# Kernel tuning notes

Measured on AMD Instinct MI355X. Metric: run time of the kernel, lower is better.

Reference implementation:

```python
import jax, jax.numpy as jnp
import numpy as np

N, E, D_IN, HEADS, C = 100000, 1600000, 128, 4, 32  # C = out_channels per head


def setup_inputs() -> dict:
    key = jax.random.key(0)
    ks = jax.random.split(key, 10)
    s = 1.0 / np.sqrt(D_IN)
    return {
        "x": jax.random.normal(ks[0], (N, D_IN), jnp.float32),
        "edge_index": jax.random.randint(ks[1], (2, E), 0, N, jnp.int64),
        "Wq": jax.random.normal(ks[2], (D_IN, HEADS * C), jnp.float32) * s,
        "bq": jnp.zeros((HEADS * C,), jnp.float32),
        "Wk": jax.random.normal(ks[3], (D_IN, HEADS * C), jnp.float32) * s,
        "bk": jnp.zeros((HEADS * C,), jnp.float32),
        "Wv": jax.random.normal(ks[4], (D_IN, HEADS * C), jnp.float32) * s,
        "bv": jnp.zeros((HEADS * C,), jnp.float32),
        "Wskip": jax.random.normal(ks[5], (D_IN, HEADS * C), jnp.float32) * s,
        "bskip": jnp.zeros((HEADS * C,), jnp.float32),
    }


def reference(x, edge_index, Wq, bq, Wk, bk, Wv, bv, Wskip, bskip):
    n = x.shape[0]
    src, dst = edge_index[0], edge_index[1]  # message flows src (j) -> dst (i)
    q = (x @ Wq + bq).reshape(n, HEADS, C)
    k = (x @ Wk + bk).reshape(n, HEADS, C)
    v = (x @ Wv + bv).reshape(n, HEADS, C)

    # per-edge attention logits [E, H]
    alpha = jnp.einsum('ehc,ehc->eh', q[dst], k[src]) / jnp.sqrt(jnp.float32(C))

    # segment softmax over incoming edges of each target node
    m = jax.ops.segment_max(alpha, dst, num_segments=n)          # [N, H]
    p = jnp.exp(alpha - m[dst])                                   # [E, H]
    z = jax.ops.segment_sum(p, dst, num_segments=n)               # [N, H]
    w = p / (z[dst] + 1e-16)                                      # [E, H]

    # softmax-weighted scatter aggregation of values
    out = jax.ops.segment_sum(v[src] * w[:, :, None], dst, num_segments=n)
    out = out.reshape(n, HEADS * C)

    # root/skip connection (beta=False default: plain add)
    out = out + x @ Wskip + bskip
    return out
```

## Files before the change

kernel.cpp:

```cpp
#include <hip/hip_runtime.h>

#define DIN 128
#define NHEADS 4
#define CH 32
#define MT 128
#define CHUNK 4096
#define NPB 256
#define EPB_IT 25

#define ST_H 136

typedef _Float16 h8 __attribute__((ext_vector_type(8)));
typedef _Float16 h2 __attribute__((ext_vector_type(2)));
typedef float f4 __attribute__((ext_vector_type(4)));
typedef unsigned int u2v __attribute__((ext_vector_type(2)));

__global__ __launch_bounds__(256) void prep_w(
    const float* __restrict__ Wq, const float* __restrict__ Wk,
    const float* __restrict__ Wv, const float* __restrict__ Wsk,
    _Float16* __restrict__ wt)
{
    int i = blockIdx.x * 256 + threadIdx.x;
    if (i >= 4 * 16384) return;
    int mat = i >> 14;
    int rem = i & 16383;
    int n  = rem >> 7;
    int kk = rem & 127;
    const float* W = (mat == 0) ? Wq : (mat == 1) ? Wk : (mat == 2) ? Wv : Wsk;
    wt[i] = (_Float16)W[kk * 128 + n];
}

__global__ __launch_bounds__(256) void qkvs_all(
    const float* __restrict__ x, const _Float16* __restrict__ wt,
    const float* __restrict__ bq, const float* __restrict__ bk,
    const float* __restrict__ bv, const float* __restrict__ bsk,
    _Float16* __restrict__ qh, _Float16* __restrict__ kvh,
    _Float16* __restrict__ skiph, int N)
{
    __shared__ _Float16 Sbuf[17408];
    const int t = threadIdx.x;
    const int rowBase = blockIdx.x * MT;

    for (int i = t; i < MT * 16; i += 256) {
        int r  = i >> 4;
        int c8 = i & 15;
        int gr = rowBase + r;
        _Float16 h[8];
        if (gr < N) {
            float4 f0 = reinterpret_cast<const float4*>(x)[(size_t)gr * 32 + c8 * 2];
            float4 f1 = reinterpret_cast<const float4*>(x)[(size_t)gr * 32 + c8 * 2 + 1];
            h[0] = (_Float16)f0.x; h[1] = (_Float16)f0.y;
            h[2] = (_Float16)f0.z; h[3] = (_Float16)f0.w;
            h[4] = (_Float16)f1.x; h[5] = (_Float16)f1.y;
            h[6] = (_Float16)f1.z; h[7] = (_Float16)f1.w;
        } else {
            #pragma unroll
            for (int j = 0; j < 8; ++j) h[j] = (_Float16)0.f;
        }
        *reinterpret_cast<uint4*>(&Sbuf[r * 128 + ((c8 ^ (r & 7)) << 3)]) =
            *reinterpret_cast<uint4*>(h);
    }
    __syncthreads();

    const int wid  = t >> 6;
    const int l    = t & 63;
    const int lm   = l & 15;
    const int quad = l >> 4;

    h8 afrag[2][4];
    #pragma unroll
    for (int kq = 0; kq < 4; ++kq) {
        int c8 = kq * 4 + quad;
        afrag[0][kq] = *reinterpret_cast<const h8*>(
            &Sbuf[(wid * 32 + lm) * 128 + ((c8 ^ (lm & 7)) << 3)]);
        afrag[1][kq] = *reinterpret_cast<const h8*>(
            &Sbuf[(wid * 32 + 16 + lm) * 128 + ((c8 ^ (lm & 7)) << 3)]);
    }
    __syncthreads();

    for (int mat = 0; mat < 4; ++mat) {
        const _Float16* __restrict__ Bsrc = wt + (size_t)mat * 16384;

        f4 acc[2][8];
        #pragma unroll
        for (int ms = 0; ms < 2; ++ms)
            #pragma unroll
            for (int nt = 0; nt < 8; ++nt)
                acc[ms][nt] = (f4){0.f, 0.f, 0.f, 0.f};

        #pragma unroll
        for (int kq = 0; kq < 4; ++kq) {
            const int k0 = (kq * 4 + quad) << 3;
            #pragma unroll
            for (int nt = 0; nt < 8; ++nt) {
                h8 b = *reinterpret_cast<const h8*>(
                    &Bsrc[(size_t)(nt * 16 + lm) * 128 + k0]);
                acc[0][nt] = __builtin_amdgcn_mfma_f32_16x16x32_f16(afrag[0][kq], b, acc[0][nt], 0, 0, 0);
                acc[1][nt] = __builtin_amdgcn_mfma_f32_16x16x32_f16(afrag[1][kq], b, acc[1][nt], 0, 0, 0);
            }
        }

        const float* bias = (mat == 0) ? bq : (mat == 1) ? bk : (mat == 2) ? bv : bsk;

        #pragma unroll
        for (int ms = 0; ms < 2; ++ms) {
            #pragma unroll
            for (int nt = 0; nt < 8; ++nt) {
                int col = nt * 16 + lm;
                float bsv = bias[col];
                int row = wid * 32 + ms * 16 + quad * 4;
                #pragma unroll
                for (int i2 = 0; i2 < 4; ++i2)
                    Sbuf[(row + i2) * ST_H + col] = (_Float16)(acc[ms][nt][i2] + bsv);
            }
        }
        __syncthreads();
        if (mat == 0 || mat == 3) {
            _Float16* __restrict__ dst = (mat == 0) ? qh : skiph;
            for (int j = t; j < 2048; j += 256) {
                int r  = j >> 4;
                int c0 = (j & 15) << 3;
                int gr = rowBase + r;
                if (gr < N)
                    *reinterpret_cast<uint4*>(&dst[(size_t)gr * 128 + c0]) =
                        *reinterpret_cast<const uint4*>(&Sbuf[r * ST_H + c0]);
            }
        } else {
            const int koff = (mat == 2) ? 4 : 0;
            for (int j = t; j < 4096; j += 256) {
                int r = j >> 5;
                int g = j & 31;
                int gr = rowBase + r;
                if (gr < N)
                    *reinterpret_cast<uint2*>(&kvh[(size_t)gr * 256 + g * 8 + koff]) =
                        *reinterpret_cast<const uint2*>(&Sbuf[r * ST_H + g * 4]);
            }
        }
        __syncthreads();
    }
}

__global__ __launch_bounds__(256) void bucket_hist(
    const int* __restrict__ ei, int* __restrict__ bcnt, int E, int nb)
{
    __shared__ int lds[512];
    for (int b = threadIdx.x; b < nb; b += 256) lds[b] = 0;
    __syncthreads();
    for (long long i = (long long)blockIdx.x * 256 + threadIdx.x; i < E;
         i += (long long)gridDim.x * 256)
        atomicAdd(&lds[ei[(size_t)E + i] >> 8], 1);
    __syncthreads();
    for (int b = threadIdx.x; b < nb; b += 256)
        if (lds[b]) atomicAdd(&bcnt[b], lds[b]);
}

__global__ __launch_bounds__(512) void scan_buckets(
    const int* __restrict__ bcnt, int* __restrict__ boff,
    int* __restrict__ bcur, int nb)
{
    __shared__ int ws[8];
    int t = threadIdx.x, lane = t & 63, wid = t >> 6;
    int v = (t < nb) ? bcnt[t] : 0;
    int s = v;
    #pragma unroll
    for (int off = 1; off < 64; off <<= 1) {
        int n = __shfl_up(s, off);
        if (lane >= off) s += n;
    }
    if (lane == 63) ws[wid] = s;
    __syncthreads();
    int add = 0;
    for (int w = 0; w < wid; ++w) add += ws[w];
    int excl = s - v + add;
    if (t < nb) { boff[t] = excl; bcur[t] = excl; }
    if (t == nb - 1) boff[nb] = excl + v;
}

__global__ __launch_bounds__(256) void bucket_scatter(
    const int* __restrict__ ei, int* __restrict__ bcur,
    uint2* __restrict__ pairs, int E, int nb)
{
    __shared__ int cnt[512];
    int t = threadIdx.x;
    for (int b = t; b < nb; b += 256) cnt[b] = 0;
    __syncthreads();

    long long e0 = (long long)blockIdx.x * (256 * EPB_IT);
    int ps[EPB_IT], pd[EPB_IT];
    #pragma unroll
    for (int j = 0; j < EPB_IT; ++j) {
        long long e = e0 + j * 256 + t;
        if (e < E) {
            ps[j] = ei[e];
            pd[j] = ei[(size_t)E + e];
            atomicAdd(&cnt[pd[j] >> 8], 1);
        } else pd[j] = -1;
    }
    __syncthreads();
    for (int b = t; b < nb; b += 256) {
        int c = cnt[b];
        if (c) cnt[b] = atomicAdd(&bcur[b], c);
    }
    __syncthreads();
    #pragma unroll
    for (int j = 0; j < EPB_IT; ++j) {
        if (pd[j] >= 0) {
            int pos = atomicAdd(&cnt[pd[j] >> 8], 1);
            pairs[pos] = make_uint2((unsigned)ps[j], (unsigned)pd[j]);
        }
    }
}

__global__ __launch_bounds__(256) void bucket_counts(
    const uint2* __restrict__ pairs, const int* __restrict__ boff,
    int* __restrict__ counts, int N)
{
    __shared__ int cnt[NPB];
    int b = blockIdx.x, t = threadIdx.x;
    cnt[t] = 0;
    __syncthreads();
    int s = boff[b], e = boff[b + 1];
    for (int i = s + t; i < e; i += 256)
        atomicAdd(&cnt[pairs[i].y & (NPB - 1)], 1);
    __syncthreads();
    int node = b * NPB + t;
    if (node < N) counts[node] = cnt[t];
}

__global__ __launch_bounds__(256) void chunk_sums(
    const int* __restrict__ counts, int* __restrict__ partials, int N)
{
    int b = blockIdx.x, t = threadIdx.x;
    int base = b * CHUNK + t * 16;
    int s = 0;
    #pragma unroll
    for (int j = 0; j < 16; ++j) {
        int i = base + j;
        if (i < N) s += counts[i];
    }
    #pragma unroll
    for (int off = 1; off < 64; off <<= 1) s += __shfl_xor(s, off);
    __shared__ int ws[4];
    int lane = t & 63, wid = t >> 6;
    if (lane == 0) ws[wid] = s;
    __syncthreads();
    if (t == 0) partials[b] = ws[0] + ws[1] + ws[2] + ws[3];
}

__global__ __launch_bounds__(256) void scan_chunks(
    const int* __restrict__ partials, int* __restrict__ chunkoff, int nch)
{
    __shared__ int ws[4];
    int t = threadIdx.x, lane = t & 63, wid = t >> 6;
    int v = (t < nch) ? partials[t] : 0;
    int s = v;
    #pragma unroll
    for (int off = 1; off < 64; off <<= 1) {
        int n = __shfl_up(s, off);
        if (lane >= off) s += n;
    }
    if (lane == 63) ws[wid] = s;
    __syncthreads();
    int add = 0;
    for (int w = 0; w < wid; ++w) add += ws[w];
    if (t < nch) chunkoff[t] = s - v + add;
}

__global__ __launch_bounds__(256) void scan_write(
    const int* __restrict__ counts, const int* __restrict__ chunkoff,
    int* __restrict__ rowptr, int N)
{
    int b = blockIdx.x, t = threadIdx.x;
    int base = b * CHUNK + t * 16;
    int vals[16];
    int s = 0;
    #pragma unroll
    for (int j = 0; j < 16; ++j) {
        int i = base + j;
        vals[j] = (i < N) ? counts[i] : 0;
        s += vals[j];
    }
    int lane = t & 63, wid = t >> 6;
    int incl = s;
    #pragma unroll
    for (int off = 1; off < 64; off <<= 1) {
        int n = __shfl_up(incl, off);
        if (lane >= off) incl += n;
    }
    __shared__ int ws[4];
    if (lane == 63) ws[wid] = incl;
    __syncthreads();
    int add = chunkoff[b];
    for (int w = 0; w < wid; ++w) add += ws[w];
    int run = incl - s + add;
    #pragma unroll
    for (int j = 0; j < 16; ++j) {
        int i = base + j;
        if (i < N) rowptr[i + 1] = run + vals[j];
        run += vals[j];
    }
    if (b == 0 && t == 0) rowptr[0] = 0;
}

__global__ __launch_bounds__(256) void bucket_place(
    const uint2* __restrict__ pairs, const int* __restrict__ boff,
    const int* __restrict__ rowptr, int* __restrict__ sorted, int N)
{
    __shared__ int cur[NPB];
    int b = blockIdx.x, t = threadIdx.x;
    int node = b * NPB + t;
    cur[t] = (node < N) ? rowptr[node] : 0;
    __syncthreads();
    int s = boff[b], e = boff[b + 1];
    for (int i = s + t; i < e; i += 256) {
        uint2 pr = pairs[i];
        int pos = atomicAdd(&cur[pr.y & (NPB - 1)], 1);
        sorted[pos] = (int)pr.x;
    }
}

__device__ inline float4 cvt4(unsigned lo, unsigned hi) {
    union { unsigned u[2]; _Float16 h[4]; } c;
    c.u[0] = lo; c.u[1] = hi;
    return make_float4((float)c.h[0], (float)c.h[1], (float)c.h[2], (float)c.h[3]);
}

__device__ inline h2 as_h2(unsigned u) {
    union { unsigned u; h2 h; } c;
    c.u = u;
    return c.h;
}

__global__ __launch_bounds__(256) void node_aggregate(
    const _Float16* __restrict__ q, const _Float16* __restrict__ kv,
    const _Float16* __restrict__ skiph,
    const int* __restrict__ rowptr, const int* __restrict__ srcs,
    float* __restrict__ out, int N)
{
    int gid  = blockIdx.x * 256 + threadIdx.x;
    int node = gid >> 5;
    if (node >= N) return;
    int l = gid & 31;

    u2v qu = __builtin_nontemporal_load(
        reinterpret_cast<const u2v*>(q + (size_t)node * 128) + l);
    h2 qa = as_h2(qu[0]), qb = as_h2(qu[1]);

    float4 acc = make_float4(0.f, 0.f, 0.f, 0.f);
    float z = 0.f;

    const uint4* kv4 = reinterpret_cast<const uint4*>(kv);
    const float SC = 0.17677669529663687f;
    int e0 = rowptr[node], e1 = rowptr[node + 1];
    int e = e0;

    for (; e + 8 <= e1; e += 8) {
        int s[8];
        #pragma unroll
        for (int j = 0; j < 8; ++j) s[j] = srcs[e + j];
        uint4 r[8];
        #pragma unroll
        for (int j = 0; j < 8; ++j) r[j] = kv4[(size_t)s[j] * 32 + l];

        float sv[8];
        #pragma unroll
        for (int j = 0; j < 8; ++j) {
            sv[j] = __builtin_amdgcn_fdot2(qa, as_h2(r[j].x),
                    __builtin_amdgcn_fdot2(qb, as_h2(r[j].y), 0.f, false), false);
        }
        #pragma unroll
        for (int j = 0; j < 8; ++j) sv[j] += __shfl_xor(sv[j], 1);
        #pragma unroll
        for (int j = 0; j < 8; ++j) sv[j] += __shfl_xor(sv[j], 2);
        #pragma unroll
        for (int j = 0; j < 8; ++j) sv[j] += __shfl_xor(sv[j], 4);

        #pragma unroll
        for (int j = 0; j < 8; ++j) {
            float p = __expf(sv[j] * SC);
            float4 v = cvt4(r[j].z, r[j].w);
            z += p;
            acc.x += p * v.x; acc.y += p * v.y;
            acc.z += p * v.z; acc.w += p * v.w;
        }
    }
    for (; e + 4 <= e1; e += 4) {
        int s0 = srcs[e], s1 = srcs[e + 1], s2 = srcs[e + 2], s3 = srcs[e + 3];
        uint4 r0 = kv4[(size_t)s0 * 32 + l];
        uint4 r1 = kv4[(size_t)s1 * 32 + l];
        uint4 r2 = kv4[(size_t)s2 * 32 + l];
        uint4 r3 = kv4[(size_t)s3 * 32 + l];
        float sa = __builtin_amdgcn_fdot2(qa, as_h2(r0.x),
                   __builtin_amdgcn_fdot2(qb, as_h2(r0.y), 0.f, false), false);
        float sb = __builtin_amdgcn_fdot2(qa, as_h2(r1.x),
                   __builtin_amdgcn_fdot2(qb, as_h2(r1.y), 0.f, false), false);
        float sc = __builtin_amdgcn_fdot2(qa, as_h2(r2.x),
                   __builtin_amdgcn_fdot2(qb, as_h2(r2.y), 0.f, false), false);
        float sd = __builtin_amdgcn_fdot2(qa, as_h2(r3.x),
                   __builtin_amdgcn_fdot2(qb, as_h2(r3.y), 0.f, false), false);
        sa += __shfl_xor(sa, 1); sb += __shfl_xor(sb, 1);
        sc += __shfl_xor(sc, 1); sd += __shfl_xor(sd, 1);
        sa += __shfl_xor(sa, 2); sb += __shfl_xor(sb, 2);
        sc += __shfl_xor(sc, 2); sd += __shfl_xor(sd, 2);
        sa += __shfl_xor(sa, 4); sb += __shfl_xor(sb, 4);
        sc += __shfl_xor(sc, 4); sd += __shfl_xor(sd, 4);
        float pa = __expf(sa * SC), pb = __expf(sb * SC);
        float pc = __expf(sc * SC), pdd = __expf(sd * SC);
        float4 v0 = cvt4(r0.z, r0.w);
        float4 v1 = cvt4(r1.z, r1.w);
        float4 v2 = cvt4(r2.z, r2.w);
        float4 v3 = cvt4(r3.z, r3.w);
        z += (pa + pb) + (pc + pdd);
        acc.x += pa * v0.x + pb * v1.x + pc * v2.x + pdd * v3.x;
        acc.y += pa * v0.y + pb * v1.y + pc * v2.y + pdd * v3.y;
        acc.z += pa * v0.z + pb * v1.z + pc * v2.z + pdd * v3.z;
        acc.w += pa * v0.w + pb * v1.w + pc * v2.w + pdd * v3.w;
    }
    for (; e < e1; ++e) {
        int s0 = srcs[e];
        uint4 r0 = kv4[(size_t)s0 * 32 + l];
        float sa = __builtin_amdgcn_fdot2(qa, as_h2(r0.x),
                   __builtin_amdgcn_fdot2(qb, as_h2(r0.y), 0.f, false), false);
        sa += __shfl_xor(sa, 1);
        sa += __shfl_xor(sa, 2);
        sa += __shfl_xor(sa, 4);
        float pa = __expf(sa * SC);
        float4 v0 = cvt4(r0.z, r0.w);
        z += pa;
        acc.x += pa * v0.x; acc.y += pa * v0.y;
        acc.z += pa * v0.z; acc.w += pa * v0.w;
    }

    u2v su = __builtin_nontemporal_load(
        reinterpret_cast<const u2v*>(skiph + (size_t)node * 128) + l);
    float4 sk = cvt4(su[0], su[1]);
    float inv = 1.f / (z + 1e-16f);
    f4 o;
    o[0] = sk.x + acc.x * inv; o[1] = sk.y + acc.y * inv;
    o[2] = sk.z + acc.z * inv; o[3] = sk.w + acc.w * inv;
    __builtin_nontemporal_store(o, reinterpret_cast<f4*>(out) + (size_t)node * 32 + l);
}

extern "C" void kernel_launch(void* const* d_in, const int* in_sizes, int n_in,
                              void* d_out, int out_size, void* d_ws, size_t ws_size,
                              hipStream_t stream)
{
    const float* x   = (const float*)d_in[0];
    const int*   ei  = (const int*)d_in[1];
    const float* Wq  = (const float*)d_in[2];
    const float* bq  = (const float*)d_in[3];
    const float* Wk  = (const float*)d_in[4];
    const float* bk  = (const float*)d_in[5];
    const float* Wv  = (const float*)d_in[6];
    const float* bv  = (const float*)d_in[7];
    const float* Wsk = (const float*)d_in[8];
    const float* bsk = (const float*)d_in[9];
    float* out = (float*)d_out;

    const int N = in_sizes[0] / DIN;
    const int E = in_sizes[1] / 2;
    const int nb = (N + NPB - 1) / NPB;

    _Float16* qh    = (_Float16*)d_ws;
    _Float16* kvh   = qh + (size_t)N * DIN;
    _Float16* skiph = kvh + (size_t)N * 256;
    _Float16* wt    = skiph + (size_t)N * DIN;
    uint2* pairs  = (uint2*)(wt + 4 * 16384);
    int* sorted   = (int*)(pairs + (size_t)E);
    int* counts   = sorted + E;
    int* rowptr   = counts + N;
    int* bcnt     = rowptr + (N + 1);
    int* boff     = bcnt + 512;
    int* bcur     = boff + 513;
    int* partials = bcur + 512;
    int* chunkoff = partials + 256;

    hipMemsetAsync(bcnt, 0, 512 * sizeof(int), stream);

    prep_w<<<(4 * 16384 + 255) / 256, 256, 0, stream>>>(Wq, Wk, Wv, Wsk, wt);

    qkvs_all<<<(N + MT - 1) / MT, 256, 0, stream>>>(x, wt, bq, bk, bv, bsk,
                                                    qh, kvh, skiph, N);

    bucket_hist<<<256, 256, 0, stream>>>(ei, bcnt, E, nb);
    scan_buckets<<<1, 512, 0, stream>>>(bcnt, boff, bcur, nb);
    int sb = (E + 256 * EPB_IT - 1) / (256 * EPB_IT);
    bucket_scatter<<<sb, 256, 0, stream>>>(ei, bcur, pairs, E, nb);
    bucket_counts<<<nb, 256, 0, stream>>>(pairs, boff, counts, N);

    int nch = (N + CHUNK - 1) / CHUNK;
    chunk_sums<<<nch, 256, 0, stream>>>(counts, partials, N);
    scan_chunks<<<1, 256, 0, stream>>>(partials, chunkoff, nch);
    scan_write<<<nch, 256, 0, stream>>>(counts, chunkoff, rowptr, N);

    bucket_place<<<nb, 256, 0, stream>>>(pairs, boff, rowptr, sorted, N);

    int ab = (N * 32 + 255) / 256;
    node_aggregate<<<ab, 256, 0, stream>>>(qh, kvh, skiph, rowptr, sorted, out, N);
}
```

Before: 414.3 us.

## Split projection kernel across weight matrices and drop nontemporal hints in aggregation

```diff
diff --git a/kernel.cpp b/kernel.cpp
--- a/kernel.cpp
+++ b/kernel.cpp
@@ -13,7 +13,6 @@
 typedef _Float16 h8 __attribute__((ext_vector_type(8)));
 typedef _Float16 h2 __attribute__((ext_vector_type(2)));
 typedef float f4 __attribute__((ext_vector_type(4)));
-typedef unsigned int u2v __attribute__((ext_vector_type(2)));
 
 __global__ __launch_bounds__(256) void prep_w(
     const float* __restrict__ Wq, const float* __restrict__ Wk,
@@ -30,7 +29,7 @@
     wt[i] = (_Float16)W[kk * 128 + n];
 }
 
-__global__ __launch_bounds__(256) void qkvs_all(
+__global__ __launch_bounds__(256) void qkvs_mat(
     const float* __restrict__ x, const _Float16* __restrict__ wt,
     const float* __restrict__ bq, const float* __restrict__ bk,
     const float* __restrict__ bv, const float* __restrict__ bsk,
@@ -39,7 +38,8 @@
 {
     __shared__ _Float16 Sbuf[17408];
     const int t = threadIdx.x;
-    const int rowBase = blockIdx.x * MT;
+    const int mat = blockIdx.x;
+    const int rowBase = blockIdx.y * MT;
 
     for (int i = t; i < MT * 16; i += 256) {
         int r  = i >> 4;
@@ -67,76 +67,69 @@
     const int lm   = l & 15;
     const int quad = l >> 4;
 
-    h8 afrag[2][4];
+    const _Float16* __restrict__ Bsrc = wt + (size_t)mat * 16384;
+
+    f4 acc[2][8];
+    #pragma unroll
+    for (int ms = 0; ms < 2; ++ms)
+        #pragma unroll
+        for (int nt = 0; nt < 8; ++nt)
+            acc[ms][nt] = (f4){0.f, 0.f, 0.f, 0.f};
+
     #pragma unroll
     for (int kq = 0; kq < 4; ++kq) {
-        int c8 = kq * 4 + quad;
-        afrag[0][kq] = *reinterpret_cast<const h8*>(
+        const int c8 = kq * 4 + quad;
+        const int k0 = c8 << 3;
+        h8 a0 = *reinterpret_cast<const h8*>(
             &Sbuf[(wid * 32 + lm) * 128 + ((c8 ^ (lm & 7)) << 3)]);
-        afrag[1][kq] = *reinterpret_cast<const h8*>(
+        h8 a1 = *reinterpret_cast<const h8*>(
             &Sbuf[(wid * 32 + 16 + lm) * 128 + ((c8 ^ (lm & 7)) << 3)]);
-    }
-    __syncthreads();
-
-    for (int mat = 0; mat < 4; ++mat) {
-        const _Float16* __restrict__ Bsrc = wt + (size_t)mat * 16384;
-
-        f4 acc[2][8];
-        #pragma unroll
-        for (int ms = 0; ms < 2; ++ms)
+        #pragma unroll
+        for (int nt = 0; nt < 8; ++nt) {
+            h8 b = *reinterpret_cast<const h8*>(
+                &Bsrc[(size_t)(nt * 16 + lm) * 128 + k0]);
+            acc[0][nt] = __builtin_amdgcn_mfma_f32_16x16x32_f16(a0, b, acc[0][nt], 0, 0, 0);
+            acc[1][nt] = __builtin_amdgcn_mfma_f32_16x16x32_f16(a1, b, acc[1][nt], 0, 0, 0);
+        }
+    }
+    __syncthreads();
+
+    const float* bias = (mat == 0) ? bq : (mat == 1) ? bk : (mat == 2) ? bv : bsk;
+
+    #pragma unroll
+    for (int ms = 0; ms < 2; ++ms) {
+        #pragma unroll
+        for (int nt = 0; nt < 8; ++nt) {
+            int col = nt * 16 + lm;
+            float bsv = bias[col];
+            int row = wid * 32 + ms * 16 + quad * 4;
             #pragma unroll
-            for (int nt = 0; nt < 8; ++nt)
-                acc[ms][nt] = (f4){0.f, 0.f, 0.f, 0.f};
-
-        #pragma unroll
-        for (int kq = 0; kq < 4; ++kq) {
-            const int k0 = (kq * 4 + quad) << 3;
-            #pragma unroll
-            for (int nt = 0; nt < 8; ++nt) {
-                h8 b = *reinterpret_cast<const h8*>(
-                    &Bsrc[(size_t)(nt * 16 + lm) * 128 + k0]);
-                acc[0][nt] = __builtin_amdgcn_mfma_f32_16x16x32_f16(afrag[0][kq], b, acc[0][nt], 0, 0, 0);
-                acc[1][nt] = __builtin_amdgcn_mfma_f32_16x16x32_f16(afrag[1][kq], b, acc[1][nt], 0, 0, 0);
-            }
-        }
-
-        const float* bias = (mat == 0) ? bq : (mat == 1) ? bk : (mat == 2) ? bv : bsk;
-
-        #pragma unroll
-        for (int ms = 0; ms < 2; ++ms) {
-            #pragma unroll
-            for (int nt = 0; nt < 8; ++nt) {
-                int col = nt * 16 + lm;
-                float bsv = bias[col];
-                int row = wid * 32 + ms * 16 + quad * 4;
-                #pragma unroll
-                for (int i2 = 0; i2 < 4; ++i2)
-                    Sbuf[(row + i2) * ST_H + col] = (_Float16)(acc[ms][nt][i2] + bsv);
-            }
-        }
-        __syncthreads();
-        if (mat == 0 || mat == 3) {
-            _Float16* __restrict__ dst = (mat == 0) ? qh : skiph;
-            for (int j = t; j < 2048; j += 256) {
-                int r  = j >> 4;
-                int c0 = (j & 15) << 3;
-                int gr = rowBase + r;
-                if (gr < N)
-                    *reinterpret_cast<uint4*>(&dst[(size_t)gr * 128 + c0]) =
-                        *reinterpret_cast<const uint4*>(&Sbuf[r * ST_H + c0]);
-            }
-        } else {
-            const int koff = (mat == 2) ? 4 : 0;
-            for (int j = t; j < 4096; j += 256) {
-                int r = j >> 5;
-                int g = j & 31;
-                int gr = rowBase + r;
-                if (gr < N)
-                    *reinterpret_cast<uint2*>(&kvh[(size_t)gr * 256 + g * 8 + koff]) =
-                        *reinterpret_cast<const uint2*>(&Sbuf[r * ST_H + g * 4]);
-            }
-        }
-        __syncthreads();
+            for (int i2 = 0; i2 < 4; ++i2)
+                Sbuf[(row + i2) * ST_H + col] = (_Float16)(acc[ms][nt][i2] + bsv);
+        }
+    }
+    __syncthreads();
+
+    if (mat == 0 || mat == 3) {
+        _Float16* __restrict__ dst = (mat == 0) ? qh : skiph;
+        for (int j = t; j < 2048; j += 256) {
+            int r  = j >> 4;
+            int c0 = (j & 15) << 3;
+            int gr = rowBase + r;
+            if (gr < N)
+                *reinterpret_cast<uint4*>(&dst[(size_t)gr * 128 + c0]) =
+                    *reinterpret_cast<const uint4*>(&Sbuf[r * ST_H + c0]);
+        }
+    } else {
+        const int koff = (mat == 2) ? 4 : 0;
+        for (int j = t; j < 4096; j += 256) {
+            int r = j >> 5;
+            int g = j & 31;
+            int gr = rowBase + r;
+            if (gr < N)
+                *reinterpret_cast<uint2*>(&kvh[(size_t)gr * 256 + g * 8 + koff]) =
+                    *reinterpret_cast<const uint2*>(&Sbuf[r * ST_H + g * 4]);
+        }
     }
 }
 
@@ -342,9 +335,8 @@
     if (node >= N) return;
     int l = gid & 31;
 
-    u2v qu = __builtin_nontemporal_load(
-        reinterpret_cast<const u2v*>(q + (size_t)node * 128) + l);
-    h2 qa = as_h2(qu[0]), qb = as_h2(qu[1]);
+    uint2 qu = reinterpret_cast<const uint2*>(q + (size_t)node * 128)[l];
+    h2 qa = as_h2(qu.x), qb = as_h2(qu.y);
 
     float4 acc = make_float4(0.f, 0.f, 0.f, 0.f);
     float z = 0.f;
@@ -431,14 +423,13 @@
         acc.z += pa * v0.z; acc.w += pa * v0.w;
     }
 
-    u2v su = __builtin_nontemporal_load(
-        reinterpret_cast<const u2v*>(skiph + (size_t)node * 128) + l);
-    float4 sk = cvt4(su[0], su[1]);
+    uint2 su = reinterpret_cast<const uint2*>(skiph + (size_t)node * 128)[l];
+    float4 sk = cvt4(su.x, su.y);
     float inv = 1.f / (z + 1e-16f);
-    f4 o;
-    o[0] = sk.x + acc.x * inv; o[1] = sk.y + acc.y * inv;
-    o[2] = sk.z + acc.z * inv; o[3] = sk.w + acc.w * inv;
-    __builtin_nontemporal_store(o, reinterpret_cast<f4*>(out) + (size_t)node * 32 + l);
+    float4 o;
+    o.x = sk.x + acc.x * inv; o.y = sk.y + acc.y * inv;
+    o.z = sk.z + acc.z * inv; o.w = sk.w + acc.w * inv;
+    reinterpret_cast<float4*>(out)[(size_t)node * 32 + l] = o;
 }
 
 extern "C" void kernel_launch(void* const* d_in, const int* in_sizes, int n_in,
@@ -479,8 +470,9 @@
 
     prep_w<<<(4 * 16384 + 255) / 256, 256, 0, stream>>>(Wq, Wk, Wv, Wsk, wt);
 
-    qkvs_all<<<(N + MT - 1) / MT, 256, 0, stream>>>(x, wt, bq, bk, bv, bsk,
-                                                    qh, kvh, skiph, N);
+    dim3 ggrid(4, (N + MT - 1) / MT);
+    qkvs_mat<<<ggrid, 256, 0, stream>>>(x, wt, bq, bk, bv, bsk,
+                                        qh, kvh, skiph, N);
 
     bucket_hist<<<256, 256, 0, stream>>>(ei, bcnt, E, nb);
     scan_buckets<<<1, 512, 0, stream>>>(bcnt, boff, bcur, nb);
```

New measurement: 413.2 us. Within noise of the previous version (-0.3%).
